# Optimization experiments

Hardware: AMD Instinct MI355X
Metric: run time of the kernel (lower is better)

## Reference

```python
import jax, jax.numpy as jnp
import numpy as np

N_EDGES, ADJ_K, EPROP_DIM = 50000, 9, 8
B, L = 512, 128
Z_DIM, T_DIM, TE_DIM, XE_DIM, H_DIM, O_DIM = 16, 48, 32, 128, 128, 32


def setup_inputs() -> dict:
    ks = jax.random.split(jax.random.key(0), 28)
    f = lambda k, s: jax.random.normal(k, s, jnp.float32) * 0.05
    in0 = Z_DIM + TE_DIM + XE_DIM + EPROP_DIM  # LSTM layer-0 input dim = 184
    mk_dim = XE_DIM + TE_DIM + EPROP_DIM       # 168
    return {
        "x": jax.random.randint(ks[0], (B, L), 0, N_EDGES),
        "dpt": jax.random.randint(ks[1], (B, L), 0, T_DIM),
        "z": jax.random.normal(ks[2], (L, B, Z_DIM), jnp.float32),
        "adj": jax.random.randint(ks[3], (N_EDGES, ADJ_K), 0, N_EDGES),
        "eprop": f(ks[4], (N_EDGES, EPROP_DIM)),
        "x_emb": f(ks[5], (N_EDGES, XE_DIM)),
        "t_emb": f(ks[6], (T_DIM, TE_DIM)),
        "tcost_emb": f(ks[7], (N_EDGES, TE_DIM)),
        "w_ih0": f(ks[8], (4 * H_DIM, in0)),
        "w_hh0": f(ks[9], (4 * H_DIM, H_DIM)),
        "b_ih0": f(ks[10], (4 * H_DIM,)),
        "b_hh0": f(ks[11], (4 * H_DIM,)),
        "w_ih1": f(ks[12], (4 * H_DIM, H_DIM)),
        "w_hh1": f(ks[13], (4 * H_DIM, H_DIM)),
        "b_ih1": f(ks[14], (4 * H_DIM,)),
        "b_hh1": f(ks[15], (4 * H_DIM,)),
        "w_ih2": f(ks[16], (4 * H_DIM, H_DIM)),
        "w_hh2": f(ks[17], (4 * H_DIM, H_DIM)),
        "b_ih2": f(ks[18], (4 * H_DIM,)),
        "b_hh2": f(ks[19], (4 * H_DIM,)),
        "wax": f(ks[20], (O_DIM, H_DIM)),
        "bax": f(ks[21], (O_DIM,)),
        "wat": f(ks[22], (O_DIM, 2 * TE_DIM)),
        "bat": f(ks[23], (O_DIM,)),
        "wmx": f(ks[24], (O_DIM, mk_dim)),
        "bmx": f(ks[25], (O_DIM,)),
        "wmt": f(ks[26], (O_DIM, mk_dim)),
        "bmt": f(ks[27], (O_DIM,)),
    }


def _lstm_cell(x, h, c, w_ih, w_hh, b_ih, b_hh):
    # PyTorch LSTMCell: gates ordered (i, f, g, o)
    g = x @ w_ih.T + b_ih + h @ w_hh.T + b_hh
    i, f, gg, o = jnp.split(g, 4, axis=-1)
    c = jax.nn.sigmoid(f) * c + jax.nn.sigmoid(i) * jnp.tanh(gg)
    h = jax.nn.sigmoid(o) * jnp.tanh(c)
    return h, c


def _forward(x, dpt, z, adj, eprop, x_emb, t_emb, tcost_emb,
             w_ih0, w_hh0, b_ih0, b_hh0, w_ih1, w_hh1, b_ih1, b_hh1,
             w_ih2, w_hh2, b_ih2, b_hh2, wax, bax, wat, bat, wmx, bmx, wmt, bmt):
    Bb = x.shape[0]
    N, K = adj.shape
    mask_id = N  # adj.size(0) + config.ADJ_MASK with ADJ_MASK=0 (pad id; never a valid node)
    H = w_hh0.shape[1]
    zro = lambda: jnp.zeros((Bb, H), x_emb.dtype)
    init = (zro(), zro(), zro(), zro(), zro(), zro())

    def step(carry, inp):
        h0, c0, h1, c1, h2, c2 = carry
        xt, dt, zt = inp                                   # [B], [B], [B,z]
        tt = t_emb[dt]                                     # [B,te]
        hid = jnp.concatenate([zt, x_emb[xt], tt, eprop[xt]], -1)
        h0, c0 = _lstm_cell(hid, h0, c0, w_ih0, w_hh0, b_ih0, b_hh0)
        h1, c1 = _lstm_cell(h0, h1, c1, w_ih1, w_hh1, b_ih1, b_hh1)
        h2, c2 = _lstm_cell(h1, h2, c2, w_ih2, w_hh2, b_ih2, b_hh2)
        afterx = jax.nn.relu(h2 @ wax.T + bax)             # [B,o]
        adjs = adj[xt]                                     # [B,K]
        ttb = jnp.broadcast_to(tt[:, None, :], (Bb, K, tt.shape[-1]))
        aftert = jax.nn.relu(jnp.concatenate([tcost_emb[adjs], ttb], -1) @ wat.T + bat)  # [B,K,o]
        mk = jnp.concatenate([x_emb[adjs], ttb, eprop[adjs]], -1)  # [B,K,xe+te+P]
        px = jnp.einsum('bo,bko->bk', afterx, mk @ wmx.T + bmx)    # [B,K]
        px = jnp.where(adjs == mask_id, -jnp.inf, px)
        pt = jnp.sum(aftert * (mk @ wmt.T + bmt), -1)              # [B,K]
        out = (jax.nn.log_softmax(px, -1), jax.nn.sigmoid(pt))
        return (h0, c0, h1, c1, h2, c2), out

    _, (pred_x, pred_t) = jax.lax.scan(step, init, (x.T, dpt.T, z))
    # torch stacks along dim 1 -> [B,L,K] then .view(-1,K)
    pred_x = jnp.transpose(pred_x, (1, 0, 2)).reshape(-1, K)
    pred_t = jnp.transpose(pred_t, (1, 0, 2)).reshape(-1, K)
    return pred_x, pred_t


def reference(x, dpt, z, adj, eprop, x_emb, t_emb, tcost_emb,
              w_ih0, w_hh0, b_ih0, b_hh0, w_ih1, w_hh1, b_ih1, b_hh1,
              w_ih2, w_hh2, b_ih2, b_hh2, wax, bax, wat, bat, wmx, bmx, wmt, bmt):
    return _forward(x, dpt, z, adj, eprop, x_emb, t_emb, tcost_emb,
                    w_ih0, w_hh0, b_ih0, b_hh0, w_ih1, w_hh1, b_ih1, b_hh1,
                    w_ih2, w_hh2, b_ih2, b_hh2, wax, bax, wat, bat, wmx, bmx, wmt, bmt)
```

## Files before the change

### kernel.cpp

```cpp
#include <hip/hip_runtime.h>
#include <hip/hip_fp16.h>
#include <math.h>
#include <stdint.h>

#define B_   512
#define L_   128
#define K_   9
#define NE   50000
#define ZD   16
#define TE   32
#define XE   128
#define EP   8
#define H_   128
#define G4   512
#define OD   32
#define IN0  184
#define MKD  168

typedef uint32_t u32;
typedef _Float16 half2v __attribute__((ext_vector_type(2)));
typedef _Float16 half8  __attribute__((ext_vector_type(8)));
typedef float    f32x4  __attribute__((ext_vector_type(4)));

__device__ __forceinline__ float sigm(float x) {
    x = fminf(fmaxf(x, -30.f), 30.f);
    return 1.f / (1.f + expf(-x));
}
__device__ __forceinline__ float tanh_f(float x) {
    x = fminf(fmaxf(x, -15.f), 15.f);
    float e = expf(2.f * x);
    return (e - 1.f) / (e + 1.f);
}
__device__ __forceinline__ float dot2f(u32 w, u32 h, float acc) {
#if __has_builtin(__builtin_amdgcn_fdot2)
    union { u32 u; half2v v; } a, b;
    a.u = w; b.u = h;
    return __builtin_amdgcn_fdot2(a.v, b.v, acc, false);
#else
    union { u32 u; __half2 h2; } a, b;
    a.u = w; b.u = h;
    float2 fa = __half22float2(a.h2), fb = __half22float2(b.h2);
    return fmaf(fa.x, fb.x, fmaf(fa.y, fb.y, acc));
#endif
}
__device__ __forceinline__ float dot4(uint4 w, uint4 h, float acc) {
    acc = dot2f(w.x, h.x, acc); acc = dot2f(w.y, h.y, acc);
    acc = dot2f(w.z, h.z, acc); acc = dot2f(w.w, h.w, acc);
    return acc;
}
__device__ __forceinline__ u32 packh(float lo, float hi) {
    union { __half2 h; u32 u; } p;
    p.h = __halves2half2(__float2half(lo), __float2half(hi));
    return p.u;
}

__global__ void __launch_bounds__(256)
kW2(const float* __restrict__ w_ih0, const float* __restrict__ w_hh0,
    const float* __restrict__ w_ih1, const float* __restrict__ w_hh1,
    const float* __restrict__ w_ih2, const float* __restrict__ w_hh2,
    const float* __restrict__ wax, const float* __restrict__ wmx,
    const float* __restrict__ wmt, const float* __restrict__ wat,
    const float* __restrict__ b_ih0, const float* __restrict__ b_hh0,
    const float* __restrict__ b_ih1, const float* __restrict__ b_hh1,
    const float* __restrict__ b_ih2, const float* __restrict__ b_hh2,
    u32* __restrict__ wsu)
{
    int gid = blockIdx.x * 256 + threadIdx.x;
    if (gid < 49152) {
        int g = gid / 96, c = gid % 96;
        wsu[gid] = (c < 92) ? packh(w_ih0[g * IN0 + 2 * c], w_ih0[g * IN0 + 2 * c + 1]) : 0u;
    } else if (gid < 81920) {
        int e = gid - 49152; int g = e >> 6, c = e & 63;
        wsu[gid] = packh(w_hh0[g * H_ + 2 * c], w_hh0[g * H_ + 2 * c + 1]);
    } else if (gid < 114688) {
        int e = gid - 81920; int g = e >> 6, c = e & 63;
        wsu[gid] = packh(w_ih1[g * H_ + 2 * c], w_ih1[g * H_ + 2 * c + 1]);
    } else if (gid < 147456) {
        int e = gid - 114688; int g = e >> 6, c = e & 63;
        wsu[gid] = packh(w_hh1[g * H_ + 2 * c], w_hh1[g * H_ + 2 * c + 1]);
    } else if (gid < 180224) {
        int e = gid - 147456; int g = e >> 6, c = e & 63;
        wsu[gid] = packh(w_ih2[g * H_ + 2 * c], w_ih2[g * H_ + 2 * c + 1]);
    } else if (gid < 212992) {
        int e = gid - 180224; int g = e >> 6, c = e & 63;
        wsu[gid] = packh(w_hh2[g * H_ + 2 * c], w_hh2[g * H_ + 2 * c + 1]);
    } else if (gid < 215040) {
        int e = gid - 212992; int o = e >> 6, c = e & 63;
        wsu[gid] = packh(wax[o * H_ + 2 * c], wax[o * H_ + 2 * c + 1]);
    } else if (gid < 217216) {
        int e = gid - 215040; int o = e / 68, c = e % 68;
        int col = c < 64 ? 2 * c : 160 + 2 * (c - 64);
        wsu[gid] = packh(wmx[o * MKD + col], wmx[o * MKD + col + 1]);
    } else if (gid < 219392) {
        int e = gid - 217216; int o = e / 68, c = e % 68;
        int col = c < 64 ? 2 * c : 160 + 2 * (c - 64);
        wsu[gid] = packh(wmt[o * MKD + col], wmt[o * MKD + col + 1]);
    } else if (gid < 219904) {
        int e = gid - 219392; int o = e >> 4, c = e & 15;
        wsu[gid] = packh(wat[o * 64 + 2 * c], wat[o * 64 + 2 * c + 1]);
    } else if (gid < 221440) {
        int e = gid - 219904; int layer = e >> 9, g = e & 511;
        float v;
        if (layer == 0)      v = b_ih0[g] + b_hh0[g];
        else if (layer == 1) v = b_ih1[g] + b_hh1[g];
        else                 v = b_ih2[g] + b_hh2[g];
        ((float*)wsu)[gid] = v;
    }
}

__global__ void __launch_bounds__(256)
kT(const float* __restrict__ t_emb,
   const float* __restrict__ wmx, const float* __restrict__ wmt,
   const float* __restrict__ wat,
   const float* __restrict__ bmx, const float* __restrict__ bmt,
   const float* __restrict__ bat, float* __restrict__ ttab)
{
    int gid = blockIdx.x * 256 + threadIdx.x;
    if (gid >= 48 * 96) return;
    int dt = gid / 96, o96 = gid % 96;
    const float* te = t_emb + dt * TE;
    int o = o96 & 31;
    float acc;
    const float* w;
    if (o96 < 32)      { acc = bmx[o]; w = wmx + o * MKD + XE; }
    else if (o96 < 64) { acc = bmt[o]; w = wmt + o * MKD + XE; }
    else               { acc = bat[o]; w = wat + o * 64 + TE; }
    for (int d = 0; d < TE; ++d) acc = fmaf(te[d], w[d], acc);
    ttab[dt * 96 + o96] = acc;
}

__global__ void __launch_bounds__(256)
kE(const float* __restrict__ x_emb, const float* __restrict__ eprop,
   const float* __restrict__ tcost,
   const u32* __restrict__ wmxp, const u32* __restrict__ wmtp,
   const u32* __restrict__ watp0, float* __restrict__ etab)
{
    __shared__ uint4 smx[544], smt[544], sat[128];
    int tid = threadIdx.x;
    for (int i = tid; i < 544; i += 256) {
        smx[i] = ((const uint4*)wmxp)[i];
        smt[i] = ((const uint4*)wmtp)[i];
    }
    if (tid < 128) sat[tid] = ((const uint4*)watp0)[tid];
    __syncthreads();
    int e = blockIdx.x * 256 + tid;
    if (e >= NE) return;

    u32 in[68], tin[16];
    const float* xr = x_emb + (size_t)e * XE;
#pragma unroll
    for (int c = 0; c < 64; ++c) in[c] = packh(xr[2 * c], xr[2 * c + 1]);
    const float* er = eprop + (size_t)e * EP;
#pragma unroll
    for (int c = 0; c < 4; ++c) in[64 + c] = packh(er[2 * c], er[2 * c + 1]);
    const float* tr = tcost + (size_t)e * TE;
#pragma unroll
    for (int c = 0; c < 16; ++c) tin[c] = packh(tr[2 * c], tr[2 * c + 1]);

    float* outp = etab + (size_t)e * 96;
    for (int o = 0; o < OD; ++o) {
        float ax = 0.f, am = 0.f, aa = 0.f;
#pragma unroll
        for (int c4 = 0; c4 < 17; ++c4) {
            uint4 wx = smx[o * 17 + c4], wt = smt[o * 17 + c4];
            ax = dot2f(wx.x, in[c4 * 4 + 0], ax);
            ax = dot2f(wx.y, in[c4 * 4 + 1], ax);
            ax = dot2f(wx.z, in[c4 * 4 + 2], ax);
            ax = dot2f(wx.w, in[c4 * 4 + 3], ax);
            am = dot2f(wt.x, in[c4 * 4 + 0], am);
            am = dot2f(wt.y, in[c4 * 4 + 1], am);
            am = dot2f(wt.z, in[c4 * 4 + 2], am);
            am = dot2f(wt.w, in[c4 * 4 + 3], am);
        }
#pragma unroll
        for (int c4 = 0; c4 < 4; ++c4) {
            uint4 wa = sat[o * 4 + c4];
            aa = dot2f(wa.x, tin[c4 * 4 + 0], aa);
            aa = dot2f(wa.y, tin[c4 * 4 + 1], aa);
            aa = dot2f(wa.z, tin[c4 * 4 + 2], aa);
            aa = dot2f(wa.w, tin[c4 * 4 + 3], aa);
        }
        outp[o] = ax; outp[32 + o] = am; outp[64 + o] = aa;
    }
}

__global__ void __launch_bounds__(512)
kAP(const int* __restrict__ x, const int* __restrict__ dpt,
    const float* __restrict__ z, const float* __restrict__ eprop,
    const float* __restrict__ x_emb, const float* __restrict__ t_emb,
    u32* __restrict__ A0)
{
    int tid = threadIdx.x;
    int i = tid >> 2, q = tid & 3;
    int bl = blockIdx.x * 128 + i;
    int xt = x[bl], dt = dpt[bl];
    int b = bl >> 7, l = bl & 127;
    const float* zr = z + ((size_t)l * B_ + b) * ZD;
    const float* xr = x_emb + (size_t)xt * XE;
    const float* tr = t_emb + (size_t)dt * TE;
    const float* er = eprop + (size_t)xt * EP;
    u32* outp = A0 + (size_t)bl * 96;
#pragma unroll
    for (int cc = 0; cc < 24; ++cc) {
        int c = q * 24 + cc;
        float lo, hi;
        if (c < 8)       { lo = zr[2 * c];          hi = zr[2 * c + 1]; }
        else if (c < 72) { lo = xr[2 * (c - 8)];    hi = xr[2 * (c - 8) + 1]; }
        else if (c < 88) { lo = tr[2 * (c - 72)];   hi = tr[2 * (c - 72) + 1]; }
        else if (c < 92) { lo = er[2 * (c - 88)];   hi = er[2 * (c - 88) + 1]; }
        else             { lo = 0.f;                hi = 0.f; }
        outp[c] = packh(lo, hi);
    }
}

template<int KC>
__global__ void __launch_bounds__(512, 2)
kGm(const _Float16* __restrict__ A, const u32* __restrict__ Wp,
    const float* __restrict__ bsum, _Float16* __restrict__ Out)
{
    const int K = KC * 32;
    int tid = threadIdx.x;
    int w = tid >> 6, l = tid & 63;
    int lr = l & 15, lq = l >> 4;
    int bl0 = blockIdx.x * 64;

    half8 a[4][KC];
#pragma unroll
    for (int t = 0; t < 4; ++t)
#pragma unroll
        for (int c = 0; c < KC; ++c)
            a[t][c] = *reinterpret_cast<const half8*>(
                A + (size_t)(bl0 + t * 16 + lr) * K + c * 32 + lq * 8);

#pragma unroll
    for (int pass = 0; pass < 4; ++pass) {
        int g = pass * 128 + w * 16 + lr;
        half8 bfr[KC];
#pragma unroll
        for (int c = 0; c < KC; ++c)
            bfr[c] = *reinterpret_cast<const half8*>(
                (const _Float16*)Wp + (size_t)g * K + c * 32 + lq * 8);
        float bias = bsum[g];
#pragma unroll
        for (int t = 0; t < 4; ++t) {
            f32x4 acc = {0.f, 0.f, 0.f, 0.f};
#pragma unroll
            for (int c = 0; c < KC; ++c)
                acc = __builtin_amdgcn_mfma_f32_16x16x32_f16(a[t][c], bfr[c], acc, 0, 0, 0);
#pragma unroll
            for (int j = 0; j < 4; ++j) {
                int item = bl0 + t * 16 + lq * 4 + j;
                Out[(size_t)item * G4 + g] = (_Float16)(acc[j] + bias);
            }
        }
    }
}

__global__ void __launch_bounds__(256, 2)
kLrec(const _Float16* __restrict__ gin, const u32* __restrict__ whp,
      _Float16* __restrict__ hout)
{
    __shared__ u32 sh[64];
    __shared__ float sg[G4];
    int t = threadIdx.x;
    int bidx = blockIdx.x;

    uint4 wA[16], wB[16];
#pragma unroll
    for (int j4 = 0; j4 < 16; ++j4) {
        wA[j4] = ((const uint4*)whp)[t * 16 + j4];
        wB[j4] = ((const uint4*)whp)[(t + 256) * 16 + j4];
    }
    if (t < 64) sh[t] = 0;
    float c_reg = 0.f;
    const _Float16* gbase = gin + (size_t)bidx * L_ * G4;
    float gA = (float)gbase[t], gB = (float)gbase[t + 256];
    __syncthreads();

    for (int l = 0; l < L_; ++l) {
        const _Float16* gnext = gbase + (size_t)(l < L_ - 1 ? l + 1 : l) * G4;
        float nA = (float)gnext[t], nB = (float)gnext[t + 256];
        float aA = gA, aB = gB;
        const uint4* shv = (const uint4*)sh;
#pragma unroll
        for (int j4 = 0; j4 < 16; ++j4) {
            uint4 hv = shv[j4];
            aA = dot4(wA[j4], hv, aA);
            aB = dot4(wB[j4], hv, aB);
        }
        sg[t] = aA; sg[t + 256] = aB;
        __syncthreads();
        if (t < 128) {
            float gi = sg[t], gf = sg[H_ + t], gg = sg[2 * H_ + t], go = sg[3 * H_ + t];
            float c = sigm(gf) * c_reg + sigm(gi) * tanh_f(gg);
            float h = sigm(go) * tanh_f(c);
            c_reg = c;
            _Float16 hh = (_Float16)h;
            ((_Float16*)sh)[t] = hh;
            hout[((size_t)bidx * L_ + l) * H_ + t] = hh;
        }
        __syncthreads();
        gA = nA; gB = nB;
    }
}

__global__ void __launch_bounds__(256)
kX2(const int* __restrict__ x, const int* __restrict__ dpt,
    const int* __restrict__ adj, const __half* __restrict__ h2seq,
    const u32* __restrict__ wap, const float* __restrict__ bax,
    const float* __restrict__ etab, const float* __restrict__ ttab,
    float* __restrict__ pred_x, float* __restrict__ pred_t)
{
    __shared__ uint4 swp[512];
    __shared__ float stt[48 * 96];
    __shared__ float sbax[32];
    int tid = threadIdx.x;
    for (int i = tid; i < 512; i += 256) swp[i] = ((const uint4*)wap)[i];
    for (int i = tid; i < 4608; i += 256) stt[i] = ttab[i];
    if (tid < 32) sbax[tid] = bax[tid];
    __syncthreads();

    int bl = blockIdx.x * 256 + tid;
    int xt = x[bl], dt = dpt[bl];

    uint4 h2r[16];
    const uint4* h2p = (const uint4*)(h2seq + (size_t)bl * H_);
#pragma unroll
    for (int q = 0; q < 16; ++q) h2r[q] = h2p[q];

    float afterx[OD];
    for (int o = 0; o < OD; ++o) {
        float acc = sbax[o];
#pragma unroll
        for (int q = 0; q < 16; ++q) {
            uint4 w = swp[o * 16 + q];
            acc = dot2f(w.x, h2r[q].x, acc);
            acc = dot2f(w.y, h2r[q].y, acc);
            acc = dot2f(w.z, h2r[q].z, acc);
            acc = dot2f(w.w, h2r[q].w, acc);
        }
        afterx[o] = acc > 0.f ? acc : 0.f;
    }

    const float4* tp = (const float4*)(stt + dt * 96);
    float px[K_];
#pragma unroll
    for (int k = 0; k < K_; ++k) {
        int a = adj[xt * K_ + k];
        int ac = a < NE ? a : 0;
        const float4* ep = (const float4*)(etab + (size_t)ac * 96);
        float sx = 0.f, st = 0.f;
#pragma unroll
        for (int q = 0; q < 8; ++q) {
            float4 e = ep[q], tt = tp[q];
            sx += afterx[q * 4 + 0] * (e.x + tt.x)
                + afterx[q * 4 + 1] * (e.y + tt.y)
                + afterx[q * 4 + 2] * (e.z + tt.z)
                + afterx[q * 4 + 3] * (e.w + tt.w);
        }
#pragma unroll
        for (int q = 0; q < 8; ++q) {
            float4 em = ep[8 + q], tm = tp[8 + q];
            float4 ea = ep[16 + q], ta = tp[16 + q];
            float at0 = fmaxf(ea.x + ta.x, 0.f);
            float at1 = fmaxf(ea.y + ta.y, 0.f);
            float at2 = fmaxf(ea.z + ta.z, 0.f);
            float at3 = fmaxf(ea.w + ta.w, 0.f);
            st += at0 * (em.x + tm.x) + at1 * (em.y + tm.y)
                + at2 * (em.z + tm.z) + at3 * (em.w + tm.w);
        }
        px[k] = (a == NE) ? -INFINITY : sx;
        pred_t[(size_t)bl * K_ + k] = 1.f / (1.f + expf(-st));
    }

    float m = px[0];
#pragma unroll
    for (int k = 1; k < K_; ++k) m = fmaxf(m, px[k]);
    float ssum = 0.f;
#pragma unroll
    for (int k = 0; k < K_; ++k) ssum += expf(px[k] - m);
    float lse = logf(ssum) + m;
#pragma unroll
    for (int k = 0; k < K_; ++k)
        pred_x[(size_t)bl * K_ + k] = px[k] - lse;
}

extern "C" void kernel_launch(void* const* d_in, const int* in_sizes, int n_in,
                              void* d_out, int out_size, void* d_ws, size_t ws_size,
                              hipStream_t stream)
{
    (void)in_sizes; (void)n_in; (void)out_size; (void)ws_size;

    const int*   x      = (const int*)  d_in[0];
    const int*   dpt    = (const int*)  d_in[1];
    const float* z      = (const float*)d_in[2];
    const int*   adj    = (const int*)  d_in[3];
    const float* eprop  = (const float*)d_in[4];
    const float* x_emb  = (const float*)d_in[5];
    const float* t_emb  = (const float*)d_in[6];
    const float* tcost  = (const float*)d_in[7];
    const float* w_ih0  = (const float*)d_in[8];
    const float* w_hh0  = (const float*)d_in[9];
    const float* b_ih0  = (const float*)d_in[10];
    const float* b_hh0  = (const float*)d_in[11];
    const float* w_ih1  = (const float*)d_in[12];
    const float* w_hh1  = (const float*)d_in[13];
    const float* b_ih1  = (const float*)d_in[14];
    const float* b_hh1  = (const float*)d_in[15];
    const float* w_ih2  = (const float*)d_in[16];
    const float* w_hh2  = (const float*)d_in[17];
    const float* b_ih2  = (const float*)d_in[18];
    const float* b_hh2  = (const float*)d_in[19];
    const float* wax    = (const float*)d_in[20];
    const float* bax    = (const float*)d_in[21];
    const float* wat    = (const float*)d_in[22];
    const float* bat    = (const float*)d_in[23];
    const float* wmx    = (const float*)d_in[24];
    const float* bmx    = (const float*)d_in[25];
    const float* wmt    = (const float*)d_in[26];
    const float* bmt    = (const float*)d_in[27];

    float* out    = (float*)d_out;
    float* pred_x = out;
    float* pred_t = out + (size_t)B_ * L_ * K_;

    u32* wsu = (u32*)d_ws;
    u32* wih0p = wsu;
    u32* whp0  = wsu + 49152;
    u32* wih1p = wsu + 81920;
    u32* whp1  = wsu + 114688;
    u32* wih2p = wsu + 147456;
    u32* whp2  = wsu + 180224;
    u32* wap   = wsu + 212992;
    u32* wmxp  = wsu + 215040;
    u32* wmtp  = wsu + 217216;
    u32* watp0 = wsu + 219392;
    float* bsum = (float*)(wsu + 219904);
    u32* A0    = wsu + 221440;
    _Float16* gin   = (_Float16*)(wsu + 6512896);
    _Float16* h0seq = (_Float16*)(wsu + 23290112);
    _Float16* h1seq = (_Float16*)(wsu + 27484416);
    _Float16* h2seq = (_Float16*)(wsu + 31678720);
    float* etab = (float*)(wsu + 35873024);
    float* ttab = (float*)(wsu + 40673024);

    kW2<<<865, 256, 0, stream>>>(w_ih0, w_hh0, w_ih1, w_hh1, w_ih2, w_hh2,
                                 wax, wmx, wmt, wat,
                                 b_ih0, b_hh0, b_ih1, b_hh1, b_ih2, b_hh2, wsu);

    kT<<<18, 256, 0, stream>>>(t_emb, wmx, wmt, wat, bmx, bmt, bat, ttab);

    kE<<<196, 256, 0, stream>>>(x_emb, eprop, tcost, wmxp, wmtp, watp0, etab);

    kAP<<<512, 512, 0, stream>>>(x, dpt, z, eprop, x_emb, t_emb, A0);

    kGm<6><<<1024, 512, 0, stream>>>((const _Float16*)A0, wih0p, bsum + 0, gin);
    kLrec<<<512, 256, 0, stream>>>(gin, whp0, h0seq);

    kGm<4><<<1024, 512, 0, stream>>>(h0seq, wih1p, bsum + 512, gin);
    kLrec<<<512, 256, 0, stream>>>(gin, whp1, h1seq);

    kGm<4><<<1024, 512, 0, stream>>>(h1seq, wih2p, bsum + 1024, gin);
    kLrec<<<512, 256, 0, stream>>>(gin, whp2, h2seq);

    kX2<<<256, 256, 0, stream>>>(x, dpt, adj, (const __half*)h2seq, wap, bax,
                                 etab, ttab, pred_x, pred_t);
}
```

Measured before the change: 933.4 us.

## Compute all four LSTM gates per thread in recurrence, one barrier per step

The recurrent LSTM kernel now uses 128 threads per sequence, each holding the W_hh rows for all four gates of one hidden unit in registers (256 VGPRs of weights). The cell update happens in the same thread, so the shared gate buffer and one of the two barriers per timestep go away. The hidden state is double-buffered in shared memory. The weight packing is reordered so these per-thread loads coalesce. In exchange, each block has half the threads with heavy register pressure and occupancy limited to one block per launch-bounds hint, which may hurt latency hiding.

New measurement: 1.020 ms. 1.09x slower.

```diff
diff --git a/kernel.cpp b/kernel.cpp
--- a/kernel.cpp
+++ b/kernel.cpp
@@ -70,19 +70,25 @@
         int g = gid / 96, c = gid % 96;
         wsu[gid] = (c < 92) ? packh(w_ih0[g * IN0 + 2 * c], w_ih0[g * IN0 + 2 * c + 1]) : 0u;
     } else if (gid < 81920) {
-        int e = gid - 49152; int g = e >> 6, c = e & 63;
+        int e = gid - 49152;
+        int q = e & 3, hd = (e >> 2) & 127, j4 = (e >> 9) & 15, g4 = e >> 13;
+        int g = g4 * 128 + hd, c = 4 * j4 + q;
         wsu[gid] = packh(w_hh0[g * H_ + 2 * c], w_hh0[g * H_ + 2 * c + 1]);
     } else if (gid < 114688) {
         int e = gid - 81920; int g = e >> 6, c = e & 63;
         wsu[gid] = packh(w_ih1[g * H_ + 2 * c], w_ih1[g * H_ + 2 * c + 1]);
     } else if (gid < 147456) {
-        int e = gid - 114688; int g = e >> 6, c = e & 63;
+        int e = gid - 114688;
+        int q = e & 3, hd = (e >> 2) & 127, j4 = (e >> 9) & 15, g4 = e >> 13;
+        int g = g4 * 128 + hd, c = 4 * j4 + q;
         wsu[gid] = packh(w_hh1[g * H_ + 2 * c], w_hh1[g * H_ + 2 * c + 1]);
     } else if (gid < 180224) {
         int e = gid - 147456; int g = e >> 6, c = e & 63;
         wsu[gid] = packh(w_ih2[g * H_ + 2 * c], w_ih2[g * H_ + 2 * c + 1]);
     } else if (gid < 212992) {
-        int e = gid - 180224; int g = e >> 6, c = e & 63;
+        int e = gid - 180224;
+        int q = e & 3, hd = (e >> 2) & 127, j4 = (e >> 9) & 15, g4 = e >> 13;
+        int g = g4 * 128 + hd, c = 4 * j4 + q;
         wsu[gid] = packh(w_hh2[g * H_ + 2 * c], w_hh2[g * H_ + 2 * c + 1]);
     } else if (gid < 215040) {
         int e = gid - 212992; int o = e >> 6, c = e & 63;
@@ -256,51 +262,57 @@
     }
 }
 
-__global__ void __launch_bounds__(256, 2)
-kLrec(const _Float16* __restrict__ gin, const u32* __restrict__ whp,
-      _Float16* __restrict__ hout)
-{
-    __shared__ u32 sh[64];
-    __shared__ float sg[G4];
-    int t = threadIdx.x;
-    int bidx = blockIdx.x;
-
-    uint4 wA[16], wB[16];
-#pragma unroll
-    for (int j4 = 0; j4 < 16; ++j4) {
-        wA[j4] = ((const uint4*)whp)[t * 16 + j4];
-        wB[j4] = ((const uint4*)whp)[(t + 256) * 16 + j4];
-    }
-    if (t < 64) sh[t] = 0;
+__global__ void __launch_bounds__(128, 1)
+kLrec2(const _Float16* __restrict__ gin, const u32* __restrict__ whr,
+       _Float16* __restrict__ hout)
+{
+    __shared__ u32 sh[2][64];
+    const int hd = threadIdx.x;
+    const int bidx = blockIdx.x;
+
+    uint4 w[4][16];
+#pragma unroll
+    for (int g4 = 0; g4 < 4; ++g4)
+#pragma unroll
+        for (int j4 = 0; j4 < 16; ++j4)
+            w[g4][j4] = ((const uint4*)whr)[(g4 * 16 + j4) * 128 + hd];
+#pragma unroll
+    for (int g4 = 0; g4 < 4; ++g4)
+#pragma unroll
+        for (int j4 = 0; j4 < 16; ++j4)
+            asm volatile("" : "+v"(w[g4][j4].x), "+v"(w[g4][j4].y),
+                              "+v"(w[g4][j4].z), "+v"(w[g4][j4].w));
+
+    if (hd < 64) sh[0][hd] = 0;
     float c_reg = 0.f;
-    const _Float16* gbase = gin + (size_t)bidx * L_ * G4;
-    float gA = (float)gbase[t], gB = (float)gbase[t + 256];
+    const _Float16* gbase = gin + (size_t)bidx * (L_ * G4);
+    float gi = (float)gbase[hd],       gf = (float)gbase[128 + hd];
+    float gg = (float)gbase[256 + hd], go = (float)gbase[384 + hd];
     __syncthreads();
 
     for (int l = 0; l < L_; ++l) {
-        const _Float16* gnext = gbase + (size_t)(l < L_ - 1 ? l + 1 : l) * G4;
-        float nA = (float)gnext[t], nB = (float)gnext[t + 256];
-        float aA = gA, aB = gB;
-        const uint4* shv = (const uint4*)sh;
+        const _Float16* gn = gbase + (size_t)(l < L_ - 1 ? l + 1 : l) * G4;
+        float ni = (float)gn[hd],       nf = (float)gn[128 + hd];
+        float ng = (float)gn[256 + hd], no = (float)gn[384 + hd];
+
+        const uint4* hv4 = (const uint4*)sh[l & 1];
+        float ai = gi, af = gf, ag = gg, ao = go;
 #pragma unroll
         for (int j4 = 0; j4 < 16; ++j4) {
-            uint4 hv = shv[j4];
-            aA = dot4(wA[j4], hv, aA);
-            aB = dot4(wB[j4], hv, aB);
-        }
-        sg[t] = aA; sg[t + 256] = aB;
+            uint4 hv = hv4[j4];
+            ai = dot4(w[0][j4], hv, ai);
+            af = dot4(w[1][j4], hv, af);
+            ag = dot4(w[2][j4], hv, ag);
+            ao = dot4(w[3][j4], hv, ao);
+        }
+        float c = sigm(af) * c_reg + sigm(ai) * tanh_f(ag);
+        float h = sigm(ao) * tanh_f(c);
+        c_reg = c;
+        _Float16 hh = (_Float16)h;
+        ((_Float16*)sh[(l + 1) & 1])[hd] = hh;
+        hout[((size_t)bidx * L_ + l) * H_ + hd] = hh;
         __syncthreads();
-        if (t < 128) {
-            float gi = sg[t], gf = sg[H_ + t], gg = sg[2 * H_ + t], go = sg[3 * H_ + t];
-            float c = sigm(gf) * c_reg + sigm(gi) * tanh_f(gg);
-            float h = sigm(go) * tanh_f(c);
-            c_reg = c;
-            _Float16 hh = (_Float16)h;
-            ((_Float16*)sh)[t] = hh;
-            hout[((size_t)bidx * L_ + l) * H_ + t] = hh;
-        }
-        __syncthreads();
-        gA = nA; gB = nB;
+        gi = ni; gf = nf; gg = ng; go = no;
     }
 }
 
@@ -426,11 +438,11 @@
 
     u32* wsu = (u32*)d_ws;
     u32* wih0p = wsu;
-    u32* whp0  = wsu + 49152;
+    u32* whr0  = wsu + 49152;
     u32* wih1p = wsu + 81920;
-    u32* whp1  = wsu + 114688;
+    u32* whr1  = wsu + 114688;
     u32* wih2p = wsu + 147456;
-    u32* whp2  = wsu + 180224;
+    u32* whr2  = wsu + 180224;
     u32* wap   = wsu + 212992;
     u32* wmxp  = wsu + 215040;
     u32* wmtp  = wsu + 217216;
@@ -455,13 +467,13 @@
     kAP<<<512, 512, 0, stream>>>(x, dpt, z, eprop, x_emb, t_emb, A0);
 
     kGm<6><<<1024, 512, 0, stream>>>((const _Float16*)A0, wih0p, bsum + 0, gin);
-    kLrec<<<512, 256, 0, stream>>>(gin, whp0, h0seq);
+    kLrec2<<<512, 128, 0, stream>>>(gin, whr0, h0seq);
 
     kGm<4><<<1024, 512, 0, stream>>>(h0seq, wih1p, bsum + 512, gin);
-    kLrec<<<512, 256, 0, stream>>>(gin, whp1, h1seq);
+    kLrec2<<<512, 128, 0, stream>>>(gin, whr1, h1seq);
 
     kGm<4><<<1024, 512, 0, stream>>>(h1seq, wih2p, bsum + 1024, gin);
-    kLrec<<<512, 256, 0, stream>>>(gin, whp2, h2seq);
+    kLrec2<<<512, 128, 0, stream>>>(gin, whr2, h2seq);
 
     kX2<<<256, 256, 0, stream>>>(x, dpt, adj, (const __half*)h2seq, wap, bax,
                                  etab, ttab, pred_x, pred_t);
```

## Batch LSTM recurrence over 16 sequences with MFMA and fuse input projection

Applied to the files above, without the earlier changes.

Replaces the per-sequence dot2 recurrence kernel with an MFMA-based kernel. Each block of 512 threads advances 16 batch rows together, with the recurrent weights held in registers and h double-buffered in LDS. For layers 1 and 2 the input-to-hidden matmul is computed inside the recurrence, which removes the separate gate-precompute GEMM launches and their global round-trip. The trade-off is a grid of only 32 blocks, so far fewer CUs are used, and each step now carries a serial chain of MFMA ops.

After: 1.288 ms. +38.0%, slower.

```diff
diff --git a/kernel.cpp b/kernel.cpp
--- a/kernel.cpp
+++ b/kernel.cpp
@@ -43,15 +43,18 @@
     return fmaf(fa.x, fb.x, fmaf(fa.y, fb.y, acc));
 #endif
 }
-__device__ __forceinline__ float dot4(uint4 w, uint4 h, float acc) {
-    acc = dot2f(w.x, h.x, acc); acc = dot2f(w.y, h.y, acc);
-    acc = dot2f(w.z, h.z, acc); acc = dot2f(w.w, h.w, acc);
-    return acc;
-}
 __device__ __forceinline__ u32 packh(float lo, float hi) {
     union { __half2 h; u32 u; } p;
     p.h = __halves2half2(__float2half(lo), __float2half(hi));
     return p.u;
+}
+__device__ __forceinline__ f32x4 cvt4h(uint2 p) {
+    union { u32 u; half2v v; } a, b;
+    a.u = p.x; b.u = p.y;
+    f32x4 r;
+    r[0] = (float)a.v[0]; r[1] = (float)a.v[1];
+    r[2] = (float)b.v[0]; r[3] = (float)b.v[1];
+    return r;
 }
 
 __global__ void __launch_bounds__(256)
@@ -256,51 +259,142 @@
     }
 }
 
-__global__ void __launch_bounds__(256, 2)
-kLrec(const _Float16* __restrict__ gin, const u32* __restrict__ whp,
-      _Float16* __restrict__ hout)
-{
-    __shared__ u32 sh[64];
-    __shared__ float sg[G4];
-    int t = threadIdx.x;
-    int bidx = blockIdx.x;
-
-    uint4 wA[16], wB[16];
-#pragma unroll
-    for (int j4 = 0; j4 < 16; ++j4) {
-        wA[j4] = ((const uint4*)whp)[t * 16 + j4];
-        wB[j4] = ((const uint4*)whp)[(t + 256) * 16 + j4];
-    }
-    if (t < 64) sh[t] = 0;
-    float c_reg = 0.f;
-    const _Float16* gbase = gin + (size_t)bidx * L_ * G4;
-    float gA = (float)gbase[t], gB = (float)gbase[t + 256];
+template<int MODE>
+__global__ void __launch_bounds__(512, 2)
+kRecM(const _Float16* __restrict__ gin, const _Float16* __restrict__ xseq,
+      const u32* __restrict__ whh, const u32* __restrict__ wih,
+      const float* __restrict__ bias, _Float16* __restrict__ hout)
+{
+    constexpr int RS = 136;
+    __shared__ _Float16 hl[2][16][RS];
+    const int tid = threadIdx.x;
+    const int w   = tid >> 6;
+    const int l   = tid & 63;
+    const int lr  = l & 15;
+    const int lq  = l >> 4;
+    const int r0  = blockIdx.x * 16;
+
+    const int tb0 = 16 * w, tb1 = 128 + 16 * w, tb2 = 256 + 16 * w, tb3 = 384 + 16 * w;
+
+    half8 ahh[4][4];
+    const _Float16* whhp = (const _Float16*)whh;
+#pragma unroll
+    for (int kc = 0; kc < 4; ++kc) {
+        ahh[0][kc] = *(const half8*)(whhp + (size_t)(tb0 + lr) * H_ + kc * 32 + lq * 8);
+        ahh[1][kc] = *(const half8*)(whhp + (size_t)(tb1 + lr) * H_ + kc * 32 + lq * 8);
+        ahh[2][kc] = *(const half8*)(whhp + (size_t)(tb2 + lr) * H_ + kc * 32 + lq * 8);
+        ahh[3][kc] = *(const half8*)(whhp + (size_t)(tb3 + lr) * H_ + kc * 32 + lq * 8);
+    }
+    half8 aih[4][4];
+    if (MODE == 1) {
+        const _Float16* wihp = (const _Float16*)wih;
+#pragma unroll
+        for (int kc = 0; kc < 4; ++kc) {
+            aih[0][kc] = *(const half8*)(wihp + (size_t)(tb0 + lr) * H_ + kc * 32 + lq * 8);
+            aih[1][kc] = *(const half8*)(wihp + (size_t)(tb1 + lr) * H_ + kc * 32 + lq * 8);
+            aih[2][kc] = *(const half8*)(wihp + (size_t)(tb2 + lr) * H_ + kc * 32 + lq * 8);
+            aih[3][kc] = *(const half8*)(wihp + (size_t)(tb3 + lr) * H_ + kc * 32 + lq * 8);
+        }
+    }
+
+    f32x4 binit[4];
+    if (MODE == 1) {
+#pragma unroll
+        for (int j = 0; j < 4; ++j) {
+            binit[0][j] = bias[tb0 + lq * 4 + j];
+            binit[1][j] = bias[tb1 + lq * 4 + j];
+            binit[2][j] = bias[tb2 + lq * 4 + j];
+            binit[3][j] = bias[tb3 + lq * 4 + j];
+        }
+    }
+
+    {
+        _Float16* hp = &hl[0][0][0];
+        for (int i = tid; i < 16 * RS; i += 512) hp[i] = (_Float16)0.f;
+    }
+
+    const _Float16* gb = (MODE == 0) ? gin + (size_t)(r0 + lr) * L_ * G4 : nullptr;
+    const _Float16* xb = (MODE == 1) ? xseq + (size_t)(r0 + lr) * L_ * H_ : nullptr;
+    uint2 gpre[4];
+    half8 bx[4];
+    if (MODE == 0) {
+        gpre[0] = *(const uint2*)(gb + tb0 + lq * 4);
+        gpre[1] = *(const uint2*)(gb + tb1 + lq * 4);
+        gpre[2] = *(const uint2*)(gb + tb2 + lq * 4);
+        gpre[3] = *(const uint2*)(gb + tb3 + lq * 4);
+    } else {
+#pragma unroll
+        for (int kc = 0; kc < 4; ++kc)
+            bx[kc] = *(const half8*)(xb + kc * 32 + lq * 8);
+    }
+
+    float c_reg[4] = {0.f, 0.f, 0.f, 0.f};
+    _Float16* houtb = hout + (size_t)(r0 + lr) * L_ * H_ + 16 * w + lq * 4;
     __syncthreads();
 
-    for (int l = 0; l < L_; ++l) {
-        const _Float16* gnext = gbase + (size_t)(l < L_ - 1 ? l + 1 : l) * G4;
-        float nA = (float)gnext[t], nB = (float)gnext[t + 256];
-        float aA = gA, aB = gB;
-        const uint4* shv = (const uint4*)sh;
-#pragma unroll
-        for (int j4 = 0; j4 < 16; ++j4) {
-            uint4 hv = shv[j4];
-            aA = dot4(wA[j4], hv, aA);
-            aB = dot4(wB[j4], hv, aB);
-        }
-        sg[t] = aA; sg[t + 256] = aB;
+    for (int t = 0; t < L_; ++t) {
+        half8 bh[4];
+#pragma unroll
+        for (int kc = 0; kc < 4; ++kc)
+            bh[kc] = *(const half8*)&hl[t & 1][lr][kc * 32 + lq * 8];
+
+        f32x4 acc[4];
+        if (MODE == 0) {
+            acc[0] = cvt4h(gpre[0]); acc[1] = cvt4h(gpre[1]);
+            acc[2] = cvt4h(gpre[2]); acc[3] = cvt4h(gpre[3]);
+        } else {
+            acc[0] = binit[0]; acc[1] = binit[1];
+            acc[2] = binit[2]; acc[3] = binit[3];
+        }
+
+        int tn = (t < L_ - 1) ? t + 1 : t;
+        uint2 gnx[4];
+        if (MODE == 0) {
+            const _Float16* gp = gb + (size_t)tn * G4;
+            gnx[0] = *(const uint2*)(gp + tb0 + lq * 4);
+            gnx[1] = *(const uint2*)(gp + tb1 + lq * 4);
+            gnx[2] = *(const uint2*)(gp + tb2 + lq * 4);
+            gnx[3] = *(const uint2*)(gp + tb3 + lq * 4);
+        }
+
+        if (MODE == 1) {
+#pragma unroll
+            for (int kc = 0; kc < 4; ++kc) {
+                acc[0] = __builtin_amdgcn_mfma_f32_16x16x32_f16(aih[0][kc], bx[kc], acc[0], 0, 0, 0);
+                acc[1] = __builtin_amdgcn_mfma_f32_16x16x32_f16(aih[1][kc], bx[kc], acc[1], 0, 0, 0);
+                acc[2] = __builtin_amdgcn_mfma_f32_16x16x32_f16(aih[2][kc], bx[kc], acc[2], 0, 0, 0);
+                acc[3] = __builtin_amdgcn_mfma_f32_16x16x32_f16(aih[3][kc], bx[kc], acc[3], 0, 0, 0);
+            }
+            const _Float16* xp = xb + (size_t)tn * H_;
+#pragma unroll
+            for (int kc = 0; kc < 4; ++kc)
+                bx[kc] = *(const half8*)(xp + kc * 32 + lq * 8);
+        }
+#pragma unroll
+        for (int kc = 0; kc < 4; ++kc) {
+            acc[0] = __builtin_amdgcn_mfma_f32_16x16x32_f16(ahh[0][kc], bh[kc], acc[0], 0, 0, 0);
+            acc[1] = __builtin_amdgcn_mfma_f32_16x16x32_f16(ahh[1][kc], bh[kc], acc[1], 0, 0, 0);
+            acc[2] = __builtin_amdgcn_mfma_f32_16x16x32_f16(ahh[2][kc], bh[kc], acc[2], 0, 0, 0);
+            acc[3] = __builtin_amdgcn_mfma_f32_16x16x32_f16(ahh[3][kc], bh[kc], acc[3], 0, 0, 0);
+        }
+
+        float hv[4];
+#pragma unroll
+        for (int j = 0; j < 4; ++j) {
+            float c = sigm(acc[1][j]) * c_reg[j] + sigm(acc[0][j]) * tanh_f(acc[2][j]);
+            hv[j] = sigm(acc[3][j]) * tanh_f(c);
+            c_reg[j] = c;
+        }
+        uint2 hp2;
+        hp2.x = packh(hv[0], hv[1]);
+        hp2.y = packh(hv[2], hv[3]);
+        *(uint2*)&hl[(t + 1) & 1][lr][16 * w + lq * 4] = hp2;
+        *(uint2*)(houtb + (size_t)t * H_) = hp2;
         __syncthreads();
-        if (t < 128) {
-            float gi = sg[t], gf = sg[H_ + t], gg = sg[2 * H_ + t], go = sg[3 * H_ + t];
-            float c = sigm(gf) * c_reg + sigm(gi) * tanh_f(gg);
-            float h = sigm(go) * tanh_f(c);
-            c_reg = c;
-            _Float16 hh = (_Float16)h;
-            ((_Float16*)sh)[t] = hh;
-            hout[((size_t)bidx * L_ + l) * H_ + t] = hh;
-        }
-        __syncthreads();
-        gA = nA; gB = nB;
+        if (MODE == 0) {
+            gpre[0] = gnx[0]; gpre[1] = gnx[1];
+            gpre[2] = gnx[2]; gpre[3] = gnx[3];
+        }
     }
 }
 
@@ -426,11 +520,11 @@
 
     u32* wsu = (u32*)d_ws;
     u32* wih0p = wsu;
-    u32* whp0  = wsu + 49152;
+    u32* whh0  = wsu + 49152;
     u32* wih1p = wsu + 81920;
-    u32* whp1  = wsu + 114688;
+    u32* whh1  = wsu + 114688;
     u32* wih2p = wsu + 147456;
-    u32* whp2  = wsu + 180224;
+    u32* whh2  = wsu + 180224;
     u32* wap   = wsu + 212992;
     u32* wmxp  = wsu + 215040;
     u32* wmtp  = wsu + 217216;
@@ -455,13 +549,10 @@
     kAP<<<512, 512, 0, stream>>>(x, dpt, z, eprop, x_emb, t_emb, A0);
 
     kGm<6><<<1024, 512, 0, stream>>>((const _Float16*)A0, wih0p, bsum + 0, gin);
-    kLrec<<<512, 256, 0, stream>>>(gin, whp0, h0seq);
-
-    kGm<4><<<1024, 512, 0, stream>>>(h0seq, wih1p, bsum + 512, gin);
-    kLrec<<<512, 256, 0, stream>>>(gin, whp1, h1seq);
-
-    kGm<4><<<1024, 512, 0, stream>>>(h1seq, wih2p, bsum + 1024, gin);
-    kLrec<<<512, 256, 0, stream>>>(gin, whp2, h2seq);
+
+    kRecM<0><<<32, 512, 0, stream>>>(gin, nullptr, whh0, nullptr, nullptr, h0seq);
+    kRecM<1><<<32, 512, 0, stream>>>(nullptr, h0seq, whh1, wih1p, bsum + 512, h1seq);
+    kRecM<1><<<32, 512, 0, stream>>>(nullptr, h1seq, whh2, wih2p, bsum + 1024, h2seq);
 
     kX2<<<256, 256, 0, stream>>>(x, dpt, adj, (const __half*)h2seq, wap, bax,
                                  etab, ttab, pred_x, pred_t);
```

## Process two batch rows per recurrent block with LDS-resident W_hh; store edge table in fp16

Applied to the files above, without the earlier changes.

The LSTM recurrence kernel now handles two batch sequences per 512-thread block. The W_hh matrix is kept in shared memory in an interleaved layout instead of in per-thread registers, so each weight fetch serves two dot products and the number of blocks is halved. Separately, the per-edge projection table is stored as fp16 rather than fp32, which halves its gather bandwidth in the output kernel at some cost in precision. The recurrence now reads 128KB of LDS on every timestep, which may become the bottleneck, and occupancy drops to one block per CU.

Result: faster. 911.4 us (-2.4%).

```diff
diff --git a/kernel.cpp b/kernel.cpp
--- a/kernel.cpp
+++ b/kernel.cpp
@@ -53,6 +53,14 @@
     p.h = __halves2half2(__float2half(lo), __float2half(hi));
     return p.u;
 }
+__device__ __forceinline__ f32x4 cvt4h(u32 a_, u32 b_) {
+    union { u32 u; half2v v; } a, b;
+    a.u = a_; b.u = b_;
+    f32x4 r;
+    r[0] = (float)a.v[0]; r[1] = (float)a.v[1];
+    r[2] = (float)b.v[0]; r[3] = (float)b.v[1];
+    return r;
+}
 
 __global__ void __launch_bounds__(256)
 kW2(const float* __restrict__ w_ih0, const float* __restrict__ w_hh0,
@@ -70,20 +78,26 @@
         int g = gid / 96, c = gid % 96;
         wsu[gid] = (c < 92) ? packh(w_ih0[g * IN0 + 2 * c], w_ih0[g * IN0 + 2 * c + 1]) : 0u;
     } else if (gid < 81920) {
-        int e = gid - 49152; int g = e >> 6, c = e & 63;
-        wsu[gid] = packh(w_hh0[g * H_ + 2 * c], w_hh0[g * H_ + 2 * c + 1]);
+        int e = gid - 49152;
+        int q = e & 3, g = (e >> 2) & 511, j4 = e >> 11;
+        int j2 = 4 * j4 + q;
+        wsu[gid] = packh(w_hh0[g * H_ + 2 * j2], w_hh0[g * H_ + 2 * j2 + 1]);
     } else if (gid < 114688) {
         int e = gid - 81920; int g = e >> 6, c = e & 63;
         wsu[gid] = packh(w_ih1[g * H_ + 2 * c], w_ih1[g * H_ + 2 * c + 1]);
     } else if (gid < 147456) {
-        int e = gid - 114688; int g = e >> 6, c = e & 63;
-        wsu[gid] = packh(w_hh1[g * H_ + 2 * c], w_hh1[g * H_ + 2 * c + 1]);
+        int e = gid - 114688;
+        int q = e & 3, g = (e >> 2) & 511, j4 = e >> 11;
+        int j2 = 4 * j4 + q;
+        wsu[gid] = packh(w_hh1[g * H_ + 2 * j2], w_hh1[g * H_ + 2 * j2 + 1]);
     } else if (gid < 180224) {
         int e = gid - 147456; int g = e >> 6, c = e & 63;
         wsu[gid] = packh(w_ih2[g * H_ + 2 * c], w_ih2[g * H_ + 2 * c + 1]);
     } else if (gid < 212992) {
-        int e = gid - 180224; int g = e >> 6, c = e & 63;
-        wsu[gid] = packh(w_hh2[g * H_ + 2 * c], w_hh2[g * H_ + 2 * c + 1]);
+        int e = gid - 180224;
+        int q = e & 3, g = (e >> 2) & 511, j4 = e >> 11;
+        int j2 = 4 * j4 + q;
+        wsu[gid] = packh(w_hh2[g * H_ + 2 * j2], w_hh2[g * H_ + 2 * j2 + 1]);
     } else if (gid < 215040) {
         int e = gid - 212992; int o = e >> 6, c = e & 63;
         wsu[gid] = packh(wax[o * H_ + 2 * c], wax[o * H_ + 2 * c + 1]);
@@ -133,7 +147,7 @@
 kE(const float* __restrict__ x_emb, const float* __restrict__ eprop,
    const float* __restrict__ tcost,
    const u32* __restrict__ wmxp, const u32* __restrict__ wmtp,
-   const u32* __restrict__ watp0, float* __restrict__ etab)
+   const u32* __restrict__ watp0, _Float16* __restrict__ etab)
 {
     __shared__ uint4 smx[544], smt[544], sat[128];
     int tid = threadIdx.x;
@@ -157,7 +171,7 @@
 #pragma unroll
     for (int c = 0; c < 16; ++c) tin[c] = packh(tr[2 * c], tr[2 * c + 1]);
 
-    float* outp = etab + (size_t)e * 96;
+    _Float16* outp = etab + (size_t)e * 96;
     for (int o = 0; o < OD; ++o) {
         float ax = 0.f, am = 0.f, aa = 0.f;
 #pragma unroll
@@ -180,7 +194,9 @@
             aa = dot2f(wa.z, tin[c4 * 4 + 2], aa);
             aa = dot2f(wa.w, tin[c4 * 4 + 3], aa);
         }
-        outp[o] = ax; outp[32 + o] = am; outp[64 + o] = aa;
+        outp[o] = (_Float16)ax;
+        outp[32 + o] = (_Float16)am;
+        outp[64 + o] = (_Float16)aa;
     }
 }
 
@@ -256,51 +272,55 @@
     }
 }
 
-__global__ void __launch_bounds__(256, 2)
-kLrec(const _Float16* __restrict__ gin, const u32* __restrict__ whp,
+__global__ void __launch_bounds__(512, 1)
+kRecL(const _Float16* __restrict__ gin, const uint4* __restrict__ whQ,
       _Float16* __restrict__ hout)
 {
-    __shared__ u32 sh[64];
-    __shared__ float sg[G4];
-    int t = threadIdx.x;
-    int bidx = blockIdx.x;
-
-    uint4 wA[16], wB[16];
-#pragma unroll
-    for (int j4 = 0; j4 < 16; ++j4) {
-        wA[j4] = ((const uint4*)whp)[t * 16 + j4];
-        wB[j4] = ((const uint4*)whp)[(t + 256) * 16 + j4];
-    }
-    if (t < 64) sh[t] = 0;
+    __shared__ uint4 wlds[16 * 512];
+    __shared__ float sg[2][G4];
+    __shared__ u32 hb[2][64];
+    const int g  = threadIdx.x;
+    const int b0 = blockIdx.x * 2;
+
+    for (int i = g; i < 16 * 512; i += 512) wlds[i] = whQ[i];
+    if (g < 128) ((u32*)hb)[g] = 0;
+
+    const int r_ = g >> 7, hd_ = g & 127;
     float c_reg = 0.f;
-    const _Float16* gbase = gin + (size_t)bidx * L_ * G4;
-    float gA = (float)gbase[t], gB = (float)gbase[t + 256];
+    const _Float16* gb0 = gin + (size_t)(b0 + 0) * L_ * G4 + g;
+    const _Float16* gb1 = gin + (size_t)(b0 + 1) * L_ * G4 + g;
+    float p0 = (float)*gb0, p1 = (float)*gb1;
     __syncthreads();
 
     for (int l = 0; l < L_; ++l) {
-        const _Float16* gnext = gbase + (size_t)(l < L_ - 1 ? l + 1 : l) * G4;
-        float nA = (float)gnext[t], nB = (float)gnext[t + 256];
-        float aA = gA, aB = gB;
-        const uint4* shv = (const uint4*)sh;
+        int ln = (l < L_ - 1) ? l + 1 : l;
+        float n0 = (float)gb0[(size_t)ln * G4];
+        float n1 = (float)gb1[(size_t)ln * G4];
+        float a0 = p0, a1 = p1;
+        const uint4* h0q = (const uint4*)hb[0];
+        const uint4* h1q = (const uint4*)hb[1];
 #pragma unroll
         for (int j4 = 0; j4 < 16; ++j4) {
-            uint4 hv = shv[j4];
-            aA = dot4(wA[j4], hv, aA);
-            aB = dot4(wB[j4], hv, aB);
-        }
-        sg[t] = aA; sg[t + 256] = aB;
+            uint4 wq  = wlds[j4 * 512 + g];
+            uint4 hq0 = h0q[j4];
+            uint4 hq1 = h1q[j4];
+            a0 = dot4(wq, hq0, a0);
+            a1 = dot4(wq, hq1, a1);
+        }
+        sg[0][g] = a0; sg[1][g] = a1;
         __syncthreads();
-        if (t < 128) {
-            float gi = sg[t], gf = sg[H_ + t], gg = sg[2 * H_ + t], go = sg[3 * H_ + t];
+        if (g < 256) {
+            float gi = sg[r_][hd_], gf = sg[r_][H_ + hd_];
+            float gg = sg[r_][2 * H_ + hd_], go = sg[r_][3 * H_ + hd_];
             float c = sigm(gf) * c_reg + sigm(gi) * tanh_f(gg);
             float h = sigm(go) * tanh_f(c);
             c_reg = c;
             _Float16 hh = (_Float16)h;
-            ((_Float16*)sh)[t] = hh;
-            hout[((size_t)bidx * L_ + l) * H_ + t] = hh;
+            ((_Float16*)hb[r_])[hd_] = hh;
+            hout[((size_t)(b0 + r_) * L_ + l) * H_ + hd_] = hh;
         }
         __syncthreads();
-        gA = nA; gB = nB;
+        p0 = n0; p1 = n1;
     }
 }
 
@@ -308,7 +328,7 @@
 kX2(const int* __restrict__ x, const int* __restrict__ dpt,
     const int* __restrict__ adj, const __half* __restrict__ h2seq,
     const u32* __restrict__ wap, const float* __restrict__ bax,
-    const float* __restrict__ etab, const float* __restrict__ ttab,
+    const _Float16* __restrict__ etab, const float* __restrict__ ttab,
     float* __restrict__ pred_x, float* __restrict__ pred_t)
 {
     __shared__ uint4 swp[512];
@@ -342,32 +362,37 @@
         afterx[o] = acc > 0.f ? acc : 0.f;
     }
 
-    const float4* tp = (const float4*)(stt + dt * 96);
+    const float* tB = stt + dt * 96;
     float px[K_];
 #pragma unroll
     for (int k = 0; k < K_; ++k) {
         int a = adj[xt * K_ + k];
         int ac = a < NE ? a : 0;
-        const float4* ep = (const float4*)(etab + (size_t)ac * 96);
+        const uint4* ep = (const uint4*)(etab + (size_t)ac * 96);
         float sx = 0.f, st = 0.f;
 #pragma unroll
-        for (int q = 0; q < 8; ++q) {
-            float4 e = ep[q], tt = tp[q];
-            sx += afterx[q * 4 + 0] * (e.x + tt.x)
-                + afterx[q * 4 + 1] * (e.y + tt.y)
-                + afterx[q * 4 + 2] * (e.z + tt.z)
-                + afterx[q * 4 + 3] * (e.w + tt.w);
-        }
-#pragma unroll
-        for (int q = 0; q < 8; ++q) {
-            float4 em = ep[8 + q], tm = tp[8 + q];
-            float4 ea = ep[16 + q], ta = tp[16 + q];
-            float at0 = fmaxf(ea.x + ta.x, 0.f);
-            float at1 = fmaxf(ea.y + ta.y, 0.f);
-            float at2 = fmaxf(ea.z + ta.z, 0.f);
-            float at3 = fmaxf(ea.w + ta.w, 0.f);
-            st += at0 * (em.x + tm.x) + at1 * (em.y + tm.y)
-                + at2 * (em.z + tm.z) + at3 * (em.w + tm.w);
+        for (int q = 0; q < 4; ++q) {
+            uint4 e = ep[q];
+            f32x4 e0 = cvt4h(e.x, e.y);
+            f32x4 e1 = cvt4h(e.z, e.w);
+#pragma unroll
+            for (int j = 0; j < 4; ++j) {
+                sx += afterx[q * 8 + j]     * (e0[j] + tB[q * 8 + j]);
+                sx += afterx[q * 8 + 4 + j] * (e1[j] + tB[q * 8 + 4 + j]);
+            }
+        }
+#pragma unroll
+        for (int q = 0; q < 4; ++q) {
+            uint4 em4 = ep[4 + q], ea4 = ep[8 + q];
+            f32x4 m0 = cvt4h(em4.x, em4.y), m1 = cvt4h(em4.z, em4.w);
+            f32x4 a0 = cvt4h(ea4.x, ea4.y), a1 = cvt4h(ea4.z, ea4.w);
+#pragma unroll
+            for (int j = 0; j < 4; ++j) {
+                float at0 = fmaxf(a0[j] + tB[64 + q * 8 + j], 0.f);
+                float at1 = fmaxf(a1[j] + tB[64 + q * 8 + 4 + j], 0.f);
+                st += at0 * (m0[j] + tB[32 + q * 8 + j]);
+                st += at1 * (m1[j] + tB[32 + q * 8 + 4 + j]);
+            }
         }
         px[k] = (a == NE) ? -INFINITY : sx;
         pred_t[(size_t)bl * K_ + k] = 1.f / (1.f + expf(-st));
@@ -426,11 +451,11 @@
 
     u32* wsu = (u32*)d_ws;
     u32* wih0p = wsu;
-    u32* whp0  = wsu + 49152;
+    u32* whhQ0 = wsu + 49152;
     u32* wih1p = wsu + 81920;
-    u32* whp1  = wsu + 114688;
+    u32* whhQ1 = wsu + 114688;
     u32* wih2p = wsu + 147456;
-    u32* whp2  = wsu + 180224;
+    u32* whhQ2 = wsu + 180224;
     u32* wap   = wsu + 212992;
     u32* wmxp  = wsu + 215040;
     u32* wmtp  = wsu + 217216;
@@ -441,7 +466,7 @@
     _Float16* h0seq = (_Float16*)(wsu + 23290112);
     _Float16* h1seq = (_Float16*)(wsu + 27484416);
     _Float16* h2seq = (_Float16*)(wsu + 31678720);
-    float* etab = (float*)(wsu + 35873024);
+    _Float16* etab  = (_Float16*)(wsu + 35873024);
     float* ttab = (float*)(wsu + 40673024);
 
     kW2<<<865, 256, 0, stream>>>(w_ih0, w_hh0, w_ih1, w_hh1, w_ih2, w_hh2,
@@ -455,13 +480,13 @@
     kAP<<<512, 512, 0, stream>>>(x, dpt, z, eprop, x_emb, t_emb, A0);
 
     kGm<6><<<1024, 512, 0, stream>>>((const _Float16*)A0, wih0p, bsum + 0, gin);
-    kLrec<<<512, 256, 0, stream>>>(gin, whp0, h0seq);
+    kRecL<<<256, 512, 0, stream>>>(gin, (const uint4*)whhQ0, h0seq);
 
     kGm<4><<<1024, 512, 0, stream>>>(h0seq, wih1p, bsum + 512, gin);
-    kLrec<<<512, 256, 0, stream>>>(gin, whp1, h1seq);
+    kRecL<<<256, 512, 0, stream>>>(gin, (const uint4*)whhQ1, h1seq);
 
     kGm<4><<<1024, 512, 0, stream>>>(h1seq, wih2p, bsum + 1024, gin);
-    kLrec<<<512, 256, 0, stream>>>(gin, whp2, h2seq);
+    kRecL<<<256, 512, 0, stream>>>(gin, (const uint4*)whhQ2, h2seq);
 
     kX2<<<256, 256, 0, stream>>>(x, dpt, adj, (const __half*)h2seq, wap, bax,
                                  etab, ttab, pred_x, pred_t);
```
